# Performance work log

Measured on AMD Instinct MI355X. Metric: run time of the kernel, lower is better.

Reference implementation:

```python
import jax, jax.numpy as jnp
import numpy as np

N_HEAD = 50000
N_TAIL = 50000
E = 1600000
IN_F = 256
OUT_F = 32
NHEAD = 4
EDGE_F = 64
N_ETYPES = 5
NEG_SLOPE = 0.2


def setup_inputs() -> dict:
    key = jax.random.key(0)
    ks = jax.random.split(key, 10)
    return {
        "head_feature": jax.random.normal(ks[0], (N_HEAD, IN_F), jnp.float32),
        "tail_feature": jax.random.normal(ks[1], (N_TAIL, IN_F), jnp.float32),
        "W": jax.random.normal(ks[2], (IN_F, OUT_F * NHEAD), jnp.float32) * 0.05,
        "W_e": jax.random.normal(ks[3], (EDGE_F, EDGE_F * NHEAD), jnp.float32) * 0.05,
        "edge_emb": jax.random.normal(ks[4], (N_ETYPES, EDGE_F), jnp.float32) * 0.1,
        "a_l": jax.random.normal(ks[5], (1, NHEAD, OUT_F), jnp.float32) * 0.1,
        "a_r": jax.random.normal(ks[6], (1, NHEAD, OUT_F), jnp.float32) * 0.1,
        "a_e": jax.random.normal(ks[7], (1, NHEAD, EDGE_F), jnp.float32) * 0.1,
        "edge_list": jax.random.randint(ks[8], (2, E), 0, N_HEAD, jnp.int64),
        "tmp_edge": jax.random.randint(ks[9], (E,), 0, N_ETYPES, jnp.int64),
    }


def reference(head_feature, tail_feature, W, W_e, edge_emb, a_l, a_r, a_e, edge_list, tmp_edge):
    n_head_nodes = head_feature.shape[0]
    nhead, out_dim = a_l.shape[1], a_l.shape[2]
    edge_feats = a_e.shape[2]

    # dense projections (dropout in eval mode = identity)
    h_head = (head_feature @ W).reshape(-1, nhead, out_dim)   # [Nh, H, D]
    h_tail = (tail_feature @ W).reshape(-1, nhead, out_dim)   # [Nt, H, D]
    e = (edge_emb @ W_e).reshape(-1, nhead, edge_feats)       # [T,  H, De]

    head_ind = edge_list[0]
    tail_ind = edge_list[1]

    # per-edge attention logits [E, H]
    h_e = (a_e * e).sum(-1)[tmp_edge]
    h_l = (a_l * h_head).sum(-1)[head_ind]
    h_r = (a_r * h_tail).sum(-1)[tail_ind]
    att = jax.nn.leaky_relu(h_l + h_r + h_e, negative_slope=NEG_SLOPE)

    # sparse softmax over dim=1 (per head-node row), per head
    m = jax.ops.segment_max(att, head_ind, num_segments=n_head_nodes)
    m = jnp.where(jnp.isfinite(m), m, jnp.zeros_like(m))  # empty rows
    ex = jnp.exp(att - m[head_ind])
    denom = jax.ops.segment_sum(ex, head_ind, num_segments=n_head_nodes)
    alpha = ex / denom[head_ind]                              # [E, H]

    # sparse-mm aggregation: out[i] = sum_e alpha_e * h_tail[tail_e]
    msg = alpha[..., None] * h_tail[tail_ind]                 # [E, H, D]
    out = jax.ops.segment_sum(msg, head_ind, num_segments=n_head_nodes)
    out = out.reshape(n_head_nodes, nhead * out_dim)
    out = jax.nn.elu(out)
    return out, alpha
```

## Files before the change

kernel.cpp:

```cpp
#include <hip/hip_runtime.h>
#include <hip/hip_bf16.h>
#include <string.h>

#define NNODE 50000
#define NEDGE 1600000
#define INF   256
#define NH    4
#define EF    64
#define NET   5

#define NBUCK 782
#define BCAP  2560
#define PBLK  391

typedef unsigned short u16t;
typedef __attribute__((ext_vector_type(8))) short short8;
typedef __attribute__((ext_vector_type(4))) float f32x4;

__device__ __forceinline__ float b2f(u16t u) {
    union { unsigned int i; float f; } v; v.i = ((unsigned int)u) << 16; return v.f;
}
__device__ __forceinline__ u16t f2b(float f) {
    __hip_bfloat16 h = __float2bfloat16(f);
    u16t u; memcpy(&u, &h, 2); return u;
}

__global__ void k_detect(const int* __restrict__ el, const int* __restrict__ ety,
                         int* __restrict__ flag) {
    int tid = threadIdx.x;
    int w = tid >> 6, lane = tid & 63;
    const int* p = (w == 0) ? el : ety;
    int x = p[2 * lane + 1];
    unsigned long long b = __ballot(x != 0);
    if (lane == 0) flag[w] = (b == 0ULL) ? 1 : 0;
}

__global__ void k_prep(const float* __restrict__ W, const float* __restrict__ We,
                       const float* __restrict__ emb, const float* __restrict__ al,
                       const float* __restrict__ ar, const float* __restrict__ ae,
                       float* __restrict__ wl, float* __restrict__ wr,
                       float* __restrict__ he) {
    __shared__ float wes[EF * NH];
    int tid = threadIdx.x;
    {
        int k = tid;
        for (int h = 0; h < NH; h++) {
            float accl = 0.f, accr = 0.f;
            for (int d = 0; d < 32; d++) {
                float w = W[k * 128 + h * 32 + d];
                accl += w * al[h * 32 + d];
                accr += w * ar[h * 32 + d];
            }
            wl[k * NH + h] = accl;
            wr[k * NH + h] = accr;
        }
    }
    if (tid < EF) {
        int k = tid;
        for (int h = 0; h < NH; h++) {
            float s = 0.f;
            for (int d = 0; d < EF; d++)
                s += We[k * (NH * EF) + h * EF + d] * ae[h * EF + d];
            wes[k * NH + h] = s;
        }
    }
    __syncthreads();
    if (tid < NET * NH) {
        int t = tid / NH, h = tid % NH;
        float s = 0.f;
        for (int k = 0; k < EF; k++)
            s += emb[t * EF + k] * wes[k * NH + h];
        he[tid] = s;
    }
}

__global__ void k_prepw(const float* __restrict__ W, u16t* __restrict__ Wfrag) {
    int idx = blockIdx.x * 256 + threadIdx.x;
    int j    = idx & 7;
    int lane = (idx >> 3) & 63;
    int ks   = (idx >> 9) & 7;
    int tile = idx >> 12;
    int n = tile * 16 + (lane & 15);
    int k = ks * 32 + (lane >> 4) * 8 + j;
    Wfrag[idx] = f2b(W[k * 128 + n]);
}

__global__ void k_fuseA(const float* __restrict__ head, const float* __restrict__ tail,
                        const float* __restrict__ wl, const float* __restrict__ wr,
                        const int* __restrict__ el, const int* __restrict__ ety,
                        const int* __restrict__ flag, int* __restrict__ cursor,
                        unsigned int* __restrict__ bucketbuf,
                        float* __restrict__ hl, float* __restrict__ hr) {
    __shared__ float w[INF * NH];
    __shared__ unsigned int srec[4096];
    __shared__ u16t sbuck[4096];
    __shared__ int hist[784];
    __shared__ int loff[784];
    __shared__ int gb[784];
    __shared__ int psum[256];
    int b = blockIdx.x;
    int tid = threadIdx.x;
    if (b < 25000) {
        int ishead = (b < 12500);
        const float* X  = ishead ? head : tail;
        const float* wv = ishead ? wl : wr;
        float* o        = ishead ? hl : hr;
        int bb          = ishead ? b : b - 12500;
        ((float4*)w)[tid] = ((const float4*)wv)[tid];
        __syncthreads();
        int wave = tid >> 6, lane = tid & 63;
        int row = bb * 4 + wave;
        float4 xv = *(const float4*)(X + (size_t)row * INF + lane * 4);
        float xs[4] = {xv.x, xv.y, xv.z, xv.w};
        float4 acc = {0.f, 0.f, 0.f, 0.f};
#pragma unroll
        for (int j = 0; j < 4; j++) {
            float xf = xs[j];
            float4 wvv = ((float4*)w)[lane * 4 + j];
            acc.x += xf * wvv.x; acc.y += xf * wvv.y;
            acc.z += xf * wvv.z; acc.w += xf * wvv.w;
        }
#pragma unroll
        for (int off = 32; off > 0; off >>= 1) {
            acc.x += __shfl_xor(acc.x, off);
            acc.y += __shfl_xor(acc.y, off);
            acc.z += __shfl_xor(acc.z, off);
            acc.w += __shfl_xor(acc.w, off);
        }
        if (lane == 0) ((float4*)o)[row] = acc;
    } else {
        int p = b - 25000;
        int base = p * 4096;
        int wf = flag[0], wt = flag[1];
        for (int i = tid; i < 784; i += 256) hist[i] = 0;
        __syncthreads();
        unsigned int rec[16];
        unsigned int br[16];
#pragma unroll
        for (int i = 0; i < 16; i++) {
            int e = base + i * 256 + tid;
            br[i] = 0xffffffffu;
            rec[i] = 0;
            if (e < NEDGE) {
                int hi = wf ? el[2 * (long long)e]           : el[e];
                int ti = wf ? el[2 * ((long long)NEDGE + e)] : el[NEDGE + e];
                int ty = wt ? ety[2 * (long long)e]          : ety[e];
                int bk = hi >> 6;
                int r = atomicAdd(&hist[bk], 1);
                rec[i] = (unsigned)ti | ((unsigned)(hi & 63) << 16) | ((unsigned)ty << 22);
                br[i]  = (unsigned)bk | ((unsigned)r << 16);
            }
        }
        __syncthreads();
        int s4[4]; int tsum = 0;
        if (tid < 196) {
#pragma unroll
            for (int j = 0; j < 4; j++) { s4[j] = hist[4 * tid + j]; tsum += s4[j]; }
        }
        psum[tid] = (tid < 196) ? tsum : 0;
        __syncthreads();
        for (int off = 1; off < 256; off <<= 1) {
            int v = (tid >= off) ? psum[tid - off] : 0;
            __syncthreads();
            psum[tid] += v;
            __syncthreads();
        }
        if (tid < 196) {
            int run = tid ? psum[tid - 1] : 0;
#pragma unroll
            for (int j = 0; j < 4; j++) {
                int bk = 4 * tid + j;
                loff[bk] = run;
                if (s4[j] > 0) gb[bk] = atomicAdd(&cursor[bk], s4[j]);
                run += s4[j];
            }
        }
        __syncthreads();
#pragma unroll
        for (int i = 0; i < 16; i++) {
            if (br[i] != 0xffffffffu) {
                int bk = br[i] & 0xffff;
                int r  = br[i] >> 16;
                int slot = loff[bk] + r;
                srec[slot] = rec[i];
                sbuck[slot] = (u16t)bk;
            }
        }
        __syncthreads();
        int tot = psum[255];
        for (int i = tid; i < tot; i += 256) {
            int bk = sbuck[i];
            int pos = gb[bk] + (i - loff[bk]);
            if (pos < BCAP) bucketbuf[(size_t)bk * BCAP + pos] = srec[i];
        }
    }
}

__global__ void k_bscan(const int* __restrict__ cursor, int* __restrict__ bstart,
                        int* __restrict__ row_start) {
    __shared__ int psum[256];
    int tid = threadIdx.x;
    int s4[4]; int tsum = 0;
    if (tid < 196) {
#pragma unroll
        for (int j = 0; j < 4; j++) {
            int bk = 4 * tid + j;
            s4[j] = (bk < NBUCK) ? cursor[bk] : 0;
            tsum += s4[j];
        }
    }
    psum[tid] = (tid < 196) ? tsum : 0;
    __syncthreads();
    for (int off = 1; off < 256; off <<= 1) {
        int v = (tid >= off) ? psum[tid - off] : 0;
        __syncthreads();
        psum[tid] += v;
        __syncthreads();
    }
    if (tid < 196) {
        int run = tid ? psum[tid - 1] : 0;
#pragma unroll
        for (int j = 0; j < 4; j++) {
            int bk = 4 * tid + j;
            if (bk < NBUCK) bstart[bk] = run;
            run += s4[j];
        }
    }
    if (tid == 255) {
        bstart[NBUCK] = psum[255];
        row_start[NNODE] = psum[255];
    }
}

__global__ void k_fuseB(const float* __restrict__ X, const u16t* __restrict__ Wfrag,
                        u16t* __restrict__ H, const unsigned int* __restrict__ bucketbuf,
                        const int* __restrict__ cursor, const int* __restrict__ bstart,
                        unsigned int* __restrict__ cpack, int* __restrict__ row_start) {
    __shared__ __attribute__((aligned(16))) u16t alds[16 * 264];
    __shared__ unsigned int lrec[BCAP];
    __shared__ unsigned int lord[BCAP];
    __shared__ int cnt[64];
    __shared__ int sc[64];
    int b = blockIdx.x;
    int tid = threadIdx.x;
    if (b < 3125) {
        int rowbase = b * 16;
        for (int i = tid; i < 1024; i += 256) {
            int row = i >> 6;
            int kc = (i & 63) * 4;
            float4 v = *(const float4*)(X + (size_t)(rowbase + row) * INF + kc);
            u16t* d = alds + row * 264 + kc;
            d[0] = f2b(v.x); d[1] = f2b(v.y); d[2] = f2b(v.z); d[3] = f2b(v.w);
        }
        __syncthreads();
        int wave = tid >> 6, lane = tid & 63;
        int m = lane & 15, quad = lane >> 4;
        int t0 = wave * 2, t1 = t0 + 1;
        f32x4 acc0 = {0.f, 0.f, 0.f, 0.f};
        f32x4 acc1 = {0.f, 0.f, 0.f, 0.f};
#pragma unroll
        for (int ks = 0; ks < 8; ks++) {
            short8 a  = *(const short8*)(alds + m * 264 + ks * 32 + quad * 8);
            short8 b0 = *(const short8*)(Wfrag + (((t0 * 8 + ks) * 64 + lane) << 3));
            short8 b1 = *(const short8*)(Wfrag + (((t1 * 8 + ks) * 64 + lane) << 3));
            acc0 = __builtin_amdgcn_mfma_f32_16x16x32_bf16(a, b0, acc0, 0, 0, 0);
            acc1 = __builtin_amdgcn_mfma_f32_16x16x32_bf16(a, b1, acc1, 0, 0, 0);
        }
        u16t* Hp = H + (size_t)rowbase * 128;
#pragma unroll
        for (int r = 0; r < 4; r++) {
            int row = quad * 4 + r;
            Hp[(size_t)row * 128 + t0 * 16 + m] = f2b(acc0[r]);
            Hp[(size_t)row * 128 + t1 * 16 + m] = f2b(acc1[r]);
        }
    } else {
        int q = b - 3125;
        int nrec = cursor[q];
        if (nrec > BCAP) nrec = BCAP;
        int bs = bstart[q];
        for (int i = tid; i < nrec; i += 256)
            lrec[i] = bucketbuf[(size_t)q * BCAP + i];
        if (tid < 64) cnt[tid] = 0;
        __syncthreads();
        unsigned int myr[10];
        int k2 = 0;
        for (int i = tid; i < nrec; i += 256) {
            int n = (lrec[i] >> 16) & 63;
            myr[k2++] = atomicAdd(&cnt[n], 1);
        }
        __syncthreads();
        if (tid < 64) sc[tid] = cnt[tid];
        __syncthreads();
        for (int off = 1; off < 64; off <<= 1) {
            int v = (tid >= off && tid < 64) ? sc[tid - off] : 0;
            __syncthreads();
            if (tid < 64) sc[tid] += v;
            __syncthreads();
        }
        k2 = 0;
        for (int i = tid; i < nrec; i += 256) {
            unsigned int rc = lrec[i];
            int n  = (rc >> 16) & 63;
            int ti = rc & 0xffff;
            int ty = rc >> 22;
            int pos = (sc[n] - cnt[n]) + (int)myr[k2++];
            lord[pos] = ((unsigned)ty << 16) | (unsigned)ti;
        }
        __syncthreads();
        for (int i = tid; i < nrec; i += 256)
            cpack[bs + i] = lord[i];
        if (tid < 64) {
            int node = q * 64 + tid;
            if (node < NNODE) row_start[node] = bs + (sc[tid] - cnt[tid]);
        }
    }
}

__global__ void k_agg(const int* __restrict__ rs, const unsigned int* __restrict__ cpack,
                      const float* __restrict__ hl, const float* __restrict__ hr,
                      const float* __restrict__ heg, const u16t* __restrict__ ht,
                      float* __restrict__ den, float2* __restrict__ out) {
    __shared__ float hes[NET * NH];
    int tid = threadIdx.x;
    if (tid < NET * NH) hes[tid] = heg[tid];
    __syncthreads();
    int wave = tid >> 6, lane = tid & 63;
    int node = blockIdx.x * 4 + wave;
    int start = rs[node], end = rs[node + 1];
    int h = lane >> 4;
    float hlv = hl[node * 4 + h];
    float a0 = 0.f, a1 = 0.f, s = 0.f;
    int j = start;
    for (; j + 4 <= end; j += 4) {
        unsigned c0 = cpack[j], c1 = cpack[j + 1], c2 = cpack[j + 2], c3 = cpack[j + 3];
        int t0 = c0 & 0xffff, t1 = c1 & 0xffff, t2 = c2 & 0xffff, t3 = c3 & 0xffff;
        float r0 = hr[t0 * 4 + h], r1 = hr[t1 * 4 + h];
        float r2 = hr[t2 * 4 + h], r3 = hr[t3 * 4 + h];
        unsigned v0 = *(const unsigned*)(ht + (size_t)t0 * 128 + lane * 2);
        unsigned v1 = *(const unsigned*)(ht + (size_t)t1 * 128 + lane * 2);
        unsigned v2 = *(const unsigned*)(ht + (size_t)t2 * 128 + lane * 2);
        unsigned v3 = *(const unsigned*)(ht + (size_t)t3 * 128 + lane * 2);
        float x0 = hlv + r0 + hes[(c0 >> 16) * 4 + h];
        float x1 = hlv + r1 + hes[(c1 >> 16) * 4 + h];
        float x2 = hlv + r2 + hes[(c2 >> 16) * 4 + h];
        float x3 = hlv + r3 + hes[(c3 >> 16) * 4 + h];
        x0 = x0 > 0.f ? x0 : 0.2f * x0;
        x1 = x1 > 0.f ? x1 : 0.2f * x1;
        x2 = x2 > 0.f ? x2 : 0.2f * x2;
        x3 = x3 > 0.f ? x3 : 0.2f * x3;
        float e0 = __expf(x0), e1 = __expf(x1), e2 = __expf(x2), e3 = __expf(x3);
        a0 += e0 * b2f((u16t)(v0 & 0xffff)) + e1 * b2f((u16t)(v1 & 0xffff))
            + e2 * b2f((u16t)(v2 & 0xffff)) + e3 * b2f((u16t)(v3 & 0xffff));
        a1 += e0 * b2f((u16t)(v0 >> 16)) + e1 * b2f((u16t)(v1 >> 16))
            + e2 * b2f((u16t)(v2 >> 16)) + e3 * b2f((u16t)(v3 >> 16));
        s  += e0 + e1 + e2 + e3;
    }
    for (; j < end; j++) {
        unsigned cp = cpack[j];
        int ti = cp & 0xffff;
        int ty = cp >> 16;
        float att = hlv + hr[ti * 4 + h] + hes[ty * 4 + h];
        att = att > 0.f ? att : 0.2f * att;
        float exv = __expf(att);
        unsigned int hv = *(const unsigned*)(ht + (size_t)ti * 128 + lane * 2);
        a0 += exv * b2f((u16t)(hv & 0xffff));
        a1 += exv * b2f((u16t)(hv >> 16));
        s  += exv;
    }
    if ((lane & 15) == 0) den[node * 4 + h] = s;
    float o0 = 0.f, o1 = 0.f;
    if (s > 0.f) { o0 = a0 / s; o1 = a1 / s; }
    o0 = o0 > 0.f ? o0 : expm1f(o0);
    o1 = o1 > 0.f ? o1 : expm1f(o1);
    float2 ov = {o0, o1};
    out[(size_t)node * 64 + lane] = ov;
}

__global__ void k_alpha(const int* __restrict__ el, const int* __restrict__ ety,
                        const int* __restrict__ flag,
                        const float* __restrict__ hl, const float* __restrict__ hr,
                        const float* __restrict__ heg, const float* __restrict__ den,
                        float* __restrict__ alpha) {
    __shared__ float hes[NET * NH];
    int tid = threadIdx.x;
    if (tid < NET * NH) hes[tid] = heg[tid];
    __syncthreads();
    int wf = flag[0], wt = flag[1];
    int e = blockIdx.x * 256 + tid;
    int hi = wf ? el[2 * (long long)e]           : el[e];
    int ti = wf ? el[2 * ((long long)NEDGE + e)] : el[NEDGE + e];
    int ty = wt ? ety[2 * (long long)e]          : ety[e];
    float4 l = ((const float4*)hl)[hi];
    float4 r = ((const float4*)hr)[ti];
    float4 d = ((const float4*)den)[hi];
    float v0 = l.x + r.x + hes[ty * 4 + 0];
    float v1 = l.y + r.y + hes[ty * 4 + 1];
    float v2 = l.z + r.z + hes[ty * 4 + 2];
    float v3 = l.w + r.w + hes[ty * 4 + 3];
    v0 = v0 > 0.f ? v0 : 0.2f * v0;
    v1 = v1 > 0.f ? v1 : 0.2f * v1;
    v2 = v2 > 0.f ? v2 : 0.2f * v2;
    v3 = v3 > 0.f ? v3 : 0.2f * v3;
    float4 o;
    o.x = d.x > 0.f ? __expf(v0) / d.x : 0.f;
    o.y = d.y > 0.f ? __expf(v1) / d.y : 0.f;
    o.z = d.z > 0.f ? __expf(v2) / d.z : 0.f;
    o.w = d.w > 0.f ? __expf(v3) / d.w : 0.f;
    ((float4*)alpha)[e] = o;
}

extern "C" void kernel_launch(void* const* d_in, const int* in_sizes, int n_in,
                              void* d_out, int out_size, void* d_ws, size_t ws_size,
                              hipStream_t stream) {
    const float* head = (const float*)d_in[0];
    const float* tail = (const float*)d_in[1];
    const float* W    = (const float*)d_in[2];
    const float* We   = (const float*)d_in[3];
    const float* emb  = (const float*)d_in[4];
    const float* al   = (const float*)d_in[5];
    const float* ar   = (const float*)d_in[6];
    const float* ae   = (const float*)d_in[7];
    const int*   el   = (const int*)d_in[8];
    const int*   ety  = (const int*)d_in[9];

    float* ws = (float*)d_ws;
    float* hl       = ws;
    float* hr       = ws + 200000;
    float* wl       = ws + 400000;
    float* wr       = ws + 401024;
    float* heg      = ws + 402048;
    int*   flag     = (int*)(ws + 402080);
    int*   bstart   = (int*)(ws + 402096);
    int*   cursor   = (int*)(ws + 402880);
    float* den      = ws + 403664;
    int*   row_start= (int*)(ws + 603664);
    u16t*  Wfrag    = (u16t*)(ws + 653668);

    float* outp   = (float*)d_out;
    float* alphap = (float*)d_out + 6400000;
    u16t*         htail = (u16t*)alphap;
    unsigned int* cpack = (unsigned int*)(alphap + 3200000);
    unsigned int* bucketbuf = (unsigned int*)outp;

    (void)hipMemsetAsync(cursor, 0, NBUCK * sizeof(int), stream);

    k_detect<<<1, 128, 0, stream>>>(el, ety, flag);
    k_prep<<<1, 256, 0, stream>>>(W, We, emb, al, ar, ae, wl, wr, heg);
    k_prepw<<<128, 256, 0, stream>>>(W, Wfrag);
    k_fuseA<<<25000 + PBLK, 256, 0, stream>>>(head, tail, wl, wr, el, ety, flag,
                                              cursor, bucketbuf, hl, hr);
    k_bscan<<<1, 256, 0, stream>>>(cursor, bstart, row_start);
    k_fuseB<<<3125 + NBUCK, 256, 0, stream>>>(tail, Wfrag, htail, bucketbuf,
                                              cursor, bstart, cpack, row_start);
    k_agg<<<NNODE / 4, 256, 0, stream>>>(row_start, cpack, hl, hr, heg, htail,
                                         den, (float2*)outp);
    k_alpha<<<NEDGE / 256, 256, 0, stream>>>(el, ety, flag, hl, hr, heg, den, alphap);
}
```

Measured before the change: 380.2 us.

## Rebalance fuseA: smaller partition blocks first, multi-row projection blocks with 16-lane reductions

The fused kernel now puts the edge-partition blocks first and halves their size (2048 edges per block, twice as many blocks), which should spread the histogram and scatter work more evenly and start it earlier. The row-projection part changes from one row per wave to 32 rows per block, with 16-lane groups each handling a row and reading the weight vector straight from global/cache instead of staging it in LDS. This cuts the block count from 25000 to about 3100 and shortens the shuffle reductions. The trade-off is fewer, heavier blocks, more atomics on the global bucket cursors, and weight reads that depend on the cache.

```diff
diff --git a/kernel.cpp b/kernel.cpp
--- a/kernel.cpp
+++ b/kernel.cpp
@@ -11,7 +11,9 @@
 
 #define NBUCK 782
 #define BCAP  2560
-#define PBLK  391
+#define EPB   2048
+#define PBLK  782
+#define RDB   1563
 
 typedef unsigned short u16t;
 typedef __attribute__((ext_vector_type(8))) short short8;
@@ -91,53 +93,23 @@
                         const int* __restrict__ flag, int* __restrict__ cursor,
                         unsigned int* __restrict__ bucketbuf,
                         float* __restrict__ hl, float* __restrict__ hr) {
-    __shared__ float w[INF * NH];
-    __shared__ unsigned int srec[4096];
-    __shared__ u16t sbuck[4096];
+    __shared__ unsigned int srec[EPB];
+    __shared__ u16t sbuck[EPB];
     __shared__ int hist[784];
     __shared__ int loff[784];
     __shared__ int gb[784];
     __shared__ int psum[256];
     int b = blockIdx.x;
     int tid = threadIdx.x;
-    if (b < 25000) {
-        int ishead = (b < 12500);
-        const float* X  = ishead ? head : tail;
-        const float* wv = ishead ? wl : wr;
-        float* o        = ishead ? hl : hr;
-        int bb          = ishead ? b : b - 12500;
-        ((float4*)w)[tid] = ((const float4*)wv)[tid];
-        __syncthreads();
-        int wave = tid >> 6, lane = tid & 63;
-        int row = bb * 4 + wave;
-        float4 xv = *(const float4*)(X + (size_t)row * INF + lane * 4);
-        float xs[4] = {xv.x, xv.y, xv.z, xv.w};
-        float4 acc = {0.f, 0.f, 0.f, 0.f};
-#pragma unroll
-        for (int j = 0; j < 4; j++) {
-            float xf = xs[j];
-            float4 wvv = ((float4*)w)[lane * 4 + j];
-            acc.x += xf * wvv.x; acc.y += xf * wvv.y;
-            acc.z += xf * wvv.z; acc.w += xf * wvv.w;
-        }
-#pragma unroll
-        for (int off = 32; off > 0; off >>= 1) {
-            acc.x += __shfl_xor(acc.x, off);
-            acc.y += __shfl_xor(acc.y, off);
-            acc.z += __shfl_xor(acc.z, off);
-            acc.w += __shfl_xor(acc.w, off);
-        }
-        if (lane == 0) ((float4*)o)[row] = acc;
-    } else {
-        int p = b - 25000;
-        int base = p * 4096;
+    if (b < PBLK) {
+        int base = b * EPB;
         int wf = flag[0], wt = flag[1];
         for (int i = tid; i < 784; i += 256) hist[i] = 0;
         __syncthreads();
-        unsigned int rec[16];
-        unsigned int br[16];
-#pragma unroll
-        for (int i = 0; i < 16; i++) {
+        unsigned int rec[8];
+        unsigned int br[8];
+#pragma unroll
+        for (int i = 0; i < 8; i++) {
             int e = base + i * 256 + tid;
             br[i] = 0xffffffffu;
             rec[i] = 0;
@@ -177,7 +149,7 @@
         }
         __syncthreads();
 #pragma unroll
-        for (int i = 0; i < 16; i++) {
+        for (int i = 0; i < 8; i++) {
             if (br[i] != 0xffffffffu) {
                 int bk = br[i] & 0xffff;
                 int r  = br[i] >> 16;
@@ -192,6 +164,51 @@
             int bk = sbuck[i];
             int pos = gb[bk] + (i - loff[bk]);
             if (pos < BCAP) bucketbuf[(size_t)bk * BCAP + pos] = srec[i];
+        }
+    } else {
+        int bb = b - PBLK;
+        int ishead = (bb < RDB);
+        const float* X  = ishead ? head : tail;
+        const float* wv = ishead ? wl : wr;
+        float* o        = ishead ? hl : hr;
+        int rowbase = (ishead ? bb : bb - RDB) * 32;
+        int wave = tid >> 6;
+        int g = (tid >> 4) & 3;
+        int l = tid & 15;
+        const float4* wv4 = (const float4*)wv;
+        float4 acc[2];
+#pragma unroll
+        for (int rr = 0; rr < 2; rr++) {
+            acc[rr].x = 0.f; acc[rr].y = 0.f; acc[rr].z = 0.f; acc[rr].w = 0.f;
+            int row = rowbase + rr * 16 + wave * 4 + g;
+            if (row < NNODE) {
+                const float* xp = X + (size_t)row * INF + l * 4;
+#pragma unroll
+                for (int c = 0; c < 4; c++) {
+                    float4 xv = *(const float4*)(xp + c * 64);
+                    float xs[4] = {xv.x, xv.y, xv.z, xv.w};
+#pragma unroll
+                    for (int j = 0; j < 4; j++) {
+                        float4 wvv = wv4[c * 64 + l * 4 + j];
+                        acc[rr].x += xs[j] * wvv.x;
+                        acc[rr].y += xs[j] * wvv.y;
+                        acc[rr].z += xs[j] * wvv.z;
+                        acc[rr].w += xs[j] * wvv.w;
+                    }
+                }
+            }
+        }
+#pragma unroll
+        for (int rr = 0; rr < 2; rr++) {
+#pragma unroll
+            for (int off = 8; off > 0; off >>= 1) {
+                acc[rr].x += __shfl_xor(acc[rr].x, off);
+                acc[rr].y += __shfl_xor(acc[rr].y, off);
+                acc[rr].z += __shfl_xor(acc[rr].z, off);
+                acc[rr].w += __shfl_xor(acc[rr].w, off);
+            }
+            int row = rowbase + rr * 16 + wave * 4 + g;
+            if (l == 0 && row < NNODE) ((float4*)o)[row] = acc[rr];
         }
     }
 }
@@ -447,8 +464,8 @@
     k_detect<<<1, 128, 0, stream>>>(el, ety, flag);
     k_prep<<<1, 256, 0, stream>>>(W, We, emb, al, ar, ae, wl, wr, heg);
     k_prepw<<<128, 256, 0, stream>>>(W, Wfrag);
-    k_fuseA<<<25000 + PBLK, 256, 0, stream>>>(head, tail, wl, wr, el, ety, flag,
-                                              cursor, bucketbuf, hl, hr);
+    k_fuseA<<<PBLK + 2 * RDB, 256, 0, stream>>>(head, tail, wl, wr, el, ety, flag,
+                                                cursor, bucketbuf, hl, hr);
     k_bscan<<<1, 256, 0, stream>>>(cursor, bstart, row_start);
     k_fuseB<<<3125 + NBUCK, 256, 0, stream>>>(tail, Wfrag, htail, bucketbuf,
                                               cursor, bstart, cpack, row_start);
```

Measured after the change: 375.5 us. Within noise of the previous version (-1.2%).
